# Performance work log

Hardware: AMD Instinct MI355X
Metric: run time of the kernel (lower is better)

The kernel has to match this reference:

```python
import jax, jax.numpy as jnp
import numpy as np

N_HEADS = 16
D_HEAD = 64
D_MODEL = 1024
CHUNK = 64
SCALE = 1.0 / np.sqrt(D_HEAD).astype(np.float32)


def binarize(x):
    # {-1,+1} with straight-through gradient (identity in bwd)
    return x + jax.lax.stop_gradient(jnp.where(x >= 0, 1.0, -1.0).astype(x.dtype) - x)


def setup_inputs() -> dict:
    key = jax.random.key(0)
    k1, k2, k3 = jax.random.split(key, 3)
    B, T, D = 2, 4096, D_MODEL
    x = jax.random.normal(k1, (B, T, D), dtype=jnp.float32)
    w_qkv = jax.random.normal(k2, (3 * D, D), dtype=jnp.float32) * (1.0 / np.sqrt(D))
    w_o = jax.random.normal(k3, (D, D), dtype=jnp.float32) * (1.0 / np.sqrt(D))
    return {"x": x, "w_qkv": w_qkv, "w_o": w_o}


def reference(x, w_qkv, w_o):
    B, T, D = x.shape
    H, d, C = N_HEADS, D_HEAD, CHUNK
    qkv = (x @ w_qkv.T).reshape(B, T, 3, H, d)
    q, k, v = qkv[:, :, 0], qkv[:, :, 1], qkv[:, :, 2]
    # -> (B, H, T, d)
    q = jnp.transpose(q, (0, 2, 1, 3)) * jnp.asarray(SCALE, x.dtype)
    k = binarize(jnp.transpose(k, (0, 2, 1, 3)))
    v = binarize(jnp.transpose(v, (0, 2, 1, 3)))

    assert T % C == 0  # T=4096 divisible by chunk=64 (pad branch not exercised)
    Nc = T // C
    qc = q.reshape(B, H, Nc, C, d)
    kc = k.reshape(B, H, Nc, C, d)
    vc = v.reshape(B, H, Nc, C, d)

    causal_mask = jnp.tril(jnp.ones((C, C), dtype=x.dtype))
    # intra-chunk: (B,H,N,C,C) scores, causal-masked, times values
    intra_scores = jnp.einsum('bhnid,bhnjd->bhnij', qc, kc) * causal_mask
    intra = jnp.einsum('bhnij,bhnjd->bhnid', intra_scores, vc)
    # per-chunk KV outer-product state: (B,H,N,d,d)
    chunk_kv = jnp.einsum('bhntk,bhntv->bhnkv', kc, vc)
    prefix = jnp.cumsum(chunk_kv, axis=2) - chunk_kv  # exclusive prefix
    cross = jnp.einsum('bhnck,bhnkv->bhncv', qc, prefix)
    output = (intra + cross).reshape(B, H, T, d)

    final_state = prefix[:, :, -1] + chunk_kv[:, :, -1]
    out = jnp.transpose(output, (0, 2, 1, 3)).reshape(B, T, D)
    return out @ w_o.T, final_state
```

## Files before the change

### kernel.cpp

```cpp
#include <hip/hip_runtime.h>

typedef __bf16 bf16;
typedef __bf16 bf16x8 __attribute__((ext_vector_type(8)));
typedef _Float16 f16;
typedef _Float16 f16x8 __attribute__((ext_vector_type(8)));
typedef float f32x4 __attribute__((ext_vector_type(4)));

#define SCALE 0.125f
#define AP 72
#define CT 128

__device__ __forceinline__ void async_ld16(const void* g, void* l) {
  __builtin_amdgcn_global_load_lds((const __attribute__((address_space(1))) void*)g,
                                   (__attribute__((address_space(3))) void*)l, 16, 0, 0);
}

__global__ __launch_bounds__(256) void k_convert(
    const float* __restrict__ x, const float* __restrict__ wqkv, const float* __restrict__ wo,
    bf16* __restrict__ xsplit, bf16* __restrict__ wsplit, f16* __restrict__ wo16)
{
  const int N1 = 2097152, N2 = 786432, N3 = 262144;
  const int i = blockIdx.x * 256 + threadIdx.x;
  if (i < N1) {
    f32x4 v = ((const f32x4*)x)[i];
    int e = i * 4, m = e >> 10, c = e & 1023;
    bf16 hi[4], lo[4];
#pragma unroll
    for (int u = 0; u < 4; ++u) { hi[u] = (bf16)v[u]; lo[u] = (bf16)(v[u] - (float)hi[u]); }
    *(ulong1*)&xsplit[(size_t)m * 2048 + c] = *(ulong1*)hi;
    *(ulong1*)&xsplit[(size_t)m * 2048 + 1024 + c] = *(ulong1*)lo;
  } else if (i < N1 + N2) {
    int j = i - N1;
    f32x4 v = ((const f32x4*)wqkv)[j];
    int e = j * 4, n = e >> 10, c = e & 1023;
    bf16 hi[4], lo[4];
#pragma unroll
    for (int u = 0; u < 4; ++u) { hi[u] = (bf16)v[u]; lo[u] = (bf16)(v[u] - (float)hi[u]); }
    *(ulong1*)&wsplit[(size_t)n * 2048 + c] = *(ulong1*)hi;
    *(ulong1*)&wsplit[(size_t)n * 2048 + 1024 + c] = *(ulong1*)lo;
  } else if (i < N1 + N2 + N3) {
    int j = i - N1 - N2;
    f32x4 v = ((const f32x4*)wo)[j];
    f16 h[4];
#pragma unroll
    for (int u = 0; u < 4; ++u) h[u] = (f16)v[u];
    *(ulong1*)&wo16[(size_t)j * 4] = *(ulong1*)h;
  }
}

__global__ __launch_bounds__(256) void k_gemm_qkv(
    const bf16* __restrict__ A, const bf16* __restrict__ B,
    bf16* __restrict__ Qws, bf16* __restrict__ Kws, bf16* __restrict__ Vws)
{
  __shared__ char smem[32768];
  const int tid = threadIdx.x;
  const int wave = tid >> 6, lane = tid & 63;
  const int quad = lane >> 4, l16 = lane & 15;
  const int bxr = (blockIdx.x < 16) ? (blockIdx.x + 8) : (blockIdx.x - 16);
  const int n0 = bxr * 128;
  const int m0 = blockIdx.y * 128;
  const int wm = (wave >> 1) << 6, wn = (wave & 1) << 6;
  const int region = n0 >> 10;
  f32x4 acc[4][4] = {};

  if (region == 0) {
    bf16* As = (bf16*)smem;
    bf16* Bs = As + 128 * 64;
    const int r8 = lane >> 3, c8 = lane & 7;
    const int sw = l16 & 7;
    const int srcoff = (c8 ^ r8) * 8;
    for (int k0 = 0; k0 < 1024; k0 += 64) {
      __syncthreads();
#pragma unroll
      for (int it = 0; it < 4; ++it) {
        const int row = wave * 32 + it * 8 + r8;
        async_ld16(A + (size_t)(m0 + row) * 2048 + k0 + srcoff, As + row * 64 + c8 * 8);
        async_ld16(B + (size_t)(n0 + row) * 2048 + k0 + srcoff, Bs + row * 64 + c8 * 8);
      }
      __syncthreads();
#pragma unroll
      for (int ks = 0; ks < 64; ks += 32) {
        bf16x8 af[4], bg[4];
#pragma unroll
        for (int mi = 0; mi < 4; ++mi)
          af[mi] = *(const bf16x8*)&As[(wm + mi * 16 + l16) * 64 + ((((ks >> 3) + quad) ^ sw) << 3)];
#pragma unroll
        for (int ni = 0; ni < 4; ++ni)
          bg[ni] = *(const bf16x8*)&Bs[(wn + ni * 16 + l16) * 64 + ((((ks >> 3) + quad) ^ sw) << 3)];
#pragma unroll
        for (int mi = 0; mi < 4; ++mi)
#pragma unroll
          for (int ni = 0; ni < 4; ++ni)
            acc[mi][ni] = __builtin_amdgcn_mfma_f32_16x16x32_bf16(af[mi], bg[ni], acc[mi][ni], 0, 0, 0);
      }
    }
  } else {
    bf16* Ah = (bf16*)smem;
    bf16* Al = Ah + 128 * 32;
    bf16* Bh = Al + 128 * 32;
    bf16* Bl = Bh + 128 * 32;
    const int rr0 = tid >> 2;
    const int sl = tid & 3;
    const int rsw = quad ^ (l16 & 3);
    for (int k0 = 0; k0 < 1024; k0 += 32) {
      __syncthreads();
#pragma unroll
      for (int rr = 0; rr < 2; ++rr) {
        const int row = rr * 64 + rr0;
        const int soff = ((sl ^ (row & 3)) << 3);
        const bf16* arow = A + (size_t)(m0 + row) * 2048 + k0 + soff;
        const bf16* brow = B + (size_t)(n0 + row) * 2048 + k0 + soff;
        bf16* ldst = (bf16*)nullptr;
        async_ld16(arow,        Ah + row * 32 + sl * 8);
        async_ld16(arow + 1024, Al + row * 32 + sl * 8);
        async_ld16(brow,        Bh + row * 32 + sl * 8);
        async_ld16(brow + 1024, Bl + row * 32 + sl * 8);
        (void)ldst;
      }
      __syncthreads();
#pragma unroll
      for (int cb = 0; cb < 3; ++cb) {
        const bf16* Asrc = (cb == 1) ? Al : Ah;
        const bf16* Bsrc = (cb == 2) ? Bl : Bh;
        bf16x8 af[4], bg[4];
#pragma unroll
        for (int mi = 0; mi < 4; ++mi)
          af[mi] = *(const bf16x8*)&Asrc[(wm + mi * 16 + l16) * 32 + (rsw << 3)];
#pragma unroll
        for (int ni = 0; ni < 4; ++ni)
          bg[ni] = *(const bf16x8*)&Bsrc[(wn + ni * 16 + l16) * 32 + (rsw << 3)];
#pragma unroll
        for (int mi = 0; mi < 4; ++mi)
#pragma unroll
          for (int ni = 0; ni < 4; ++ni)
            acc[mi][ni] = __builtin_amdgcn_mfma_f32_16x16x32_bf16(af[mi], bg[ni], acc[mi][ni], 0, 0, 0);
      }
    }
  }

  bf16* Ct = (bf16*)smem;
  __syncthreads();
#pragma unroll
  for (int mi = 0; mi < 4; ++mi) {
    const int ml = wm + mi * 16 + quad * 4;
#pragma unroll
    for (int ni = 0; ni < 4; ++ni) {
      const int nl = wn + ni * 16 + l16;
#pragma unroll
      for (int r = 0; r < 4; ++r) {
        const float v = acc[mi][ni][r];
        bf16 o;
        if (region == 0) o = (bf16)(v * SCALE);
        else             o = (bf16)((v >= 0.f) ? 1.f : -1.f);
        Ct[(ml + r) * CT + nl] = o;
      }
    }
  }
  __syncthreads();
  {
    const int row = tid >> 1, half = tid & 1;
    const int nn = (n0 & 1023) + half * 64;
    const int h = nn >> 6;
    const int b = m0 >> 12, t = (m0 & 4095) + row;
    bf16* base = (region == 0) ? Qws : (region == 1) ? Kws : Vws;
    bf16* dst = base + ((size_t)(b * 16 + h) * 4096 + t) * 64;
    const bf16* src = &Ct[row * CT + half * 64];
#pragma unroll
    for (int u = 0; u < 8; ++u)
      *(bf16x8*)(dst + u * 8) = *(const bf16x8*)(src + u * 8);
  }
}

__global__ __launch_bounds__(256) void k_ckv(
    const bf16* __restrict__ Kws, const bf16* __restrict__ Vws, float* __restrict__ ckv)
{
  __shared__ bf16 Kt[64 * AP];
  __shared__ bf16 Vt[64 * AP];
  const int tid = threadIdx.x;
  const int nchunk = blockIdx.x & 63, bh = blockIdx.x >> 6;
  const size_t tbase = ((size_t)bh * 4096 + (size_t)nchunk * 64) * 64;
  const int row = tid >> 2, c0 = (tid & 3) << 4;
  {
    const bf16x8* gk = (const bf16x8*)(Kws + tbase + row * 64 + c0);
    const bf16x8* gv = (const bf16x8*)(Vws + tbase + row * 64 + c0);
    bf16x8 k0 = gk[0], k1 = gk[1], v0 = gv[0], v1 = gv[1];
#pragma unroll
    for (int u = 0; u < 8; ++u) {
      Kt[(c0 + u) * AP + row] = k0[u];
      Kt[(c0 + 8 + u) * AP + row] = k1[u];
      Vt[(c0 + u) * AP + row] = v0[u];
      Vt[(c0 + 8 + u) * AP + row] = v1[u];
    }
  }
  __syncthreads();
  const int wave = tid >> 6, lane = tid & 63;
  const int quad = lane >> 4, l16 = lane & 15;
  const int ti = wave;
  bf16x8 ka[2];
#pragma unroll
  for (int kk = 0; kk < 2; ++kk)
    ka[kk] = *(const bf16x8*)&Kt[(ti * 16 + l16) * AP + kk * 32 + quad * 8];
  float* dst = ckv + ((size_t)bh * 64 + nchunk) * 4096;
#pragma unroll
  for (int td = 0; td < 4; ++td) {
    f32x4 acc = {};
#pragma unroll
    for (int kk = 0; kk < 2; ++kk) {
      const bf16x8 vb = *(const bf16x8*)&Vt[(td * 16 + l16) * AP + kk * 32 + quad * 8];
      acc = __builtin_amdgcn_mfma_f32_16x16x32_bf16(ka[kk], vb, acc, 0, 0, 0);
    }
#pragma unroll
    for (int r = 0; r < 4; ++r)
      dst[(ti * 16 + quad * 4 + r) * 64 + td * 16 + l16] = acc[r];
  }
}

__global__ __launch_bounds__(256) void k_scan(float* __restrict__ ckv, float* __restrict__ fin)
{
  const int idx = blockIdx.x * 256 + threadIdx.x;
  float* p = ckv + ((size_t)(idx >> 12)) * 64 * 4096 + (idx & 4095);
  float run = 0.f;
#pragma unroll
  for (int n = 0; n < 64; ++n) {
    const float v = p[(size_t)n * 4096];
    p[(size_t)n * 4096] = run;
    run += v;
  }
  fin[idx] = run;
}

__global__ __launch_bounds__(256) void k_attn(
    const bf16* __restrict__ Qws, const bf16* __restrict__ Kws, const bf16* __restrict__ Vws,
    const float* __restrict__ pref, f16* __restrict__ attn)
{
  __shared__ bf16 Qs[64 * AP];
  __shared__ bf16 Ks[64 * AP];
  __shared__ bf16 Vt[64 * AP];
  __shared__ bf16 Ph[64 * AP];
  __shared__ bf16 Pl[64 * AP];
  __shared__ bf16 Ss[64 * AP];
  const int tid = threadIdx.x;
  const int blk = blockIdx.x;
  const int nchunk = blk & 63, bh = blk >> 6;
  const int b = bh >> 4, h = bh & 15;
  const size_t tbase = ((size_t)bh * 4096 + (size_t)nchunk * 64) * 64;
  const int row = tid >> 2, c0 = (tid & 3) << 4;
  {
    const bf16x8* gq = (const bf16x8*)(Qws + tbase + row * 64 + c0);
    *(bf16x8*)&Qs[row * AP + c0] = gq[0];
    *(bf16x8*)&Qs[row * AP + c0 + 8] = gq[1];
    const bf16x8* gk = (const bf16x8*)(Kws + tbase + row * 64 + c0);
    *(bf16x8*)&Ks[row * AP + c0] = gk[0];
    *(bf16x8*)&Ks[row * AP + c0 + 8] = gk[1];
    const bf16x8* gv = (const bf16x8*)(Vws + tbase + row * 64 + c0);
    bf16x8 v0 = gv[0], v1 = gv[1];
#pragma unroll
    for (int u = 0; u < 8; ++u) {
      Vt[(c0 + u) * AP + row] = v0[u];
      Vt[(c0 + 8 + u) * AP + row] = v1[u];
    }
    const float* gp = pref + ((size_t)bh * 64 + nchunk) * 4096 + row * 64 + c0;
#pragma unroll
    for (int u = 0; u < 16; ++u) {
      const float p = gp[u];
      const bf16 hi = (bf16)p;
      Ph[(c0 + u) * AP + row] = hi;
      Pl[(c0 + u) * AP + row] = (bf16)(p - (float)hi);
    }
  }
  __syncthreads();

  const int wave = tid >> 6, lane = tid & 63;
  const int quad = lane >> 4, l16 = lane & 15;
  const int ti = wave;

  bf16x8 qa[2];
#pragma unroll
  for (int kk = 0; kk < 2; ++kk)
    qa[kk] = *(const bf16x8*)&Qs[(ti * 16 + l16) * AP + kk * 32 + quad * 8];

  f32x4 sacc[4] = {};
#pragma unroll
  for (int tj = 0; tj < 4; ++tj)
#pragma unroll
    for (int kk = 0; kk < 2; ++kk) {
      const bf16x8 kb = *(const bf16x8*)&Ks[(tj * 16 + l16) * AP + kk * 32 + quad * 8];
      sacc[tj] = __builtin_amdgcn_mfma_f32_16x16x32_bf16(qa[kk], kb, sacc[tj], 0, 0, 0);
    }
#pragma unroll
  for (int tj = 0; tj < 4; ++tj)
#pragma unroll
    for (int r = 0; r < 4; ++r) {
      const int i = ti * 16 + quad * 4 + r;
      const int jj = tj * 16 + l16;
      Ss[i * AP + jj] = (bf16)((jj <= i) ? sacc[tj][r] : 0.f);
    }
  __syncthreads();

  bf16x8 sa[2];
#pragma unroll
  for (int kk = 0; kk < 2; ++kk)
    sa[kk] = *(const bf16x8*)&Ss[(ti * 16 + l16) * AP + kk * 32 + quad * 8];
  f32x4 oacc[4] = {};
#pragma unroll
  for (int td = 0; td < 4; ++td) {
#pragma unroll
    for (int kk = 0; kk < 2; ++kk) {
      const bf16x8 vb = *(const bf16x8*)&Vt[(td * 16 + l16) * AP + kk * 32 + quad * 8];
      oacc[td] = __builtin_amdgcn_mfma_f32_16x16x32_bf16(sa[kk], vb, oacc[td], 0, 0, 0);
    }
#pragma unroll
    for (int kk = 0; kk < 2; ++kk) {
      const bf16x8 pb = *(const bf16x8*)&Ph[(td * 16 + l16) * AP + kk * 32 + quad * 8];
      oacc[td] = __builtin_amdgcn_mfma_f32_16x16x32_bf16(qa[kk], pb, oacc[td], 0, 0, 0);
      const bf16x8 pb2 = *(const bf16x8*)&Pl[(td * 16 + l16) * AP + kk * 32 + quad * 8];
      oacc[td] = __builtin_amdgcn_mfma_f32_16x16x32_bf16(qa[kk], pb2, oacc[td], 0, 0, 0);
    }
  }
  __syncthreads();
  f16* Os = (f16*)Ss;
#pragma unroll
  for (int td = 0; td < 4; ++td)
#pragma unroll
    for (int r = 0; r < 4; ++r) {
      const int i = ti * 16 + quad * 4 + r;
      const int dd = td * 16 + l16;
      Os[i * AP + dd] = (f16)oacc[td][r];
    }
  __syncthreads();
  {
    const int i2 = tid >> 2, q4 = tid & 3;
    const int t = nchunk * 64 + i2;
    f16* dst = attn + ((size_t)(b * 4096 + t)) * 1024 + h * 64 + q4 * 16;
    const f16* src = &Os[i2 * AP + q4 * 16];
    *(f16x8*)(dst) = *(const f16x8*)(src);
    *(f16x8*)(dst + 8) = *(const f16x8*)(src + 8);
  }
}

__global__ __launch_bounds__(256) void k_gemm_out(
    const f16* __restrict__ A, const f16* __restrict__ B, float* __restrict__ out)
{
  __shared__ f16 As[128 * 64];
  __shared__ f16 Bs[128 * 64];
  const int tid = threadIdx.x;
  const int wave = tid >> 6, lane = tid & 63;
  const int quad = lane >> 4, l16 = lane & 15;
  const int n0 = blockIdx.x * 128;
  const int m0 = blockIdx.y * 128;
  const int wm = (wave >> 1) << 6, wn = (wave & 1) << 6;
  const int r8 = lane >> 3, c8 = lane & 7;
  const int sw = l16 & 7;
  const int srcoff = (c8 ^ r8) * 8;
  f32x4 acc[4][4] = {};

  for (int k0 = 0; k0 < 1024; k0 += 64) {
    __syncthreads();
#pragma unroll
    for (int it = 0; it < 4; ++it) {
      const int row = wave * 32 + it * 8 + r8;
      async_ld16(A + (size_t)(m0 + row) * 1024 + k0 + srcoff, As + row * 64 + c8 * 8);
      async_ld16(B + (size_t)(n0 + row) * 1024 + k0 + srcoff, Bs + row * 64 + c8 * 8);
    }
    __syncthreads();
#pragma unroll
    for (int ks = 0; ks < 64; ks += 32) {
      f16x8 af[4], bg[4];
#pragma unroll
      for (int mi = 0; mi < 4; ++mi)
        af[mi] = *(const f16x8*)&As[(wm + mi * 16 + l16) * 64 + ((((ks >> 3) + quad) ^ sw) << 3)];
#pragma unroll
      for (int ni = 0; ni < 4; ++ni)
        bg[ni] = *(const f16x8*)&Bs[(wn + ni * 16 + l16) * 64 + ((((ks >> 3) + quad) ^ sw) << 3)];
#pragma unroll
      for (int mi = 0; mi < 4; ++mi)
#pragma unroll
        for (int ni = 0; ni < 4; ++ni)
          acc[mi][ni] = __builtin_amdgcn_mfma_f32_16x16x32_f16(af[mi], bg[ni], acc[mi][ni], 0, 0, 0);
    }
  }
#pragma unroll
  for (int mi = 0; mi < 4; ++mi)
#pragma unroll
    for (int ni = 0; ni < 4; ++ni)
#pragma unroll
      for (int r = 0; r < 4; ++r) {
        const int m = m0 + wm + mi * 16 + quad * 4 + r;
        const int n = n0 + wn + ni * 16 + l16;
        out[(size_t)m * 1024 + n] = acc[mi][ni][r];
      }
}

extern "C" void kernel_launch(void* const* d_in, const int* in_sizes, int n_in,
                              void* d_out, int out_size, void* d_ws, size_t ws_size,
                              hipStream_t stream)
{
  const float* x = (const float*)d_in[0];
  const float* wqkv = (const float*)d_in[1];
  const float* wo = (const float*)d_in[2];
  float* out = (float*)d_out;
  char* ws = (char*)d_ws;

  bf16* xsplit = (bf16*)(ws);
  bf16* wsplit = (bf16*)(ws + 33554432);
  f16*  wo16   = (f16*)(ws + 46137344);
  bf16* Qws    = (bf16*)(ws + 48234496);
  bf16* Kws    = (bf16*)(ws + 65011712);
  bf16* Vws    = (bf16*)(ws + 81788928);
  float* ckv   = (float*)(ws + 98566144);
  f16*  attn   = (f16*)(ws + 132120576);
  float* fin   = out + 8388608;

  k_convert<<<12288, 256, 0, stream>>>(x, wqkv, wo, xsplit, wsplit, wo16);
  k_gemm_qkv<<<dim3(24, 64), 256, 0, stream>>>(xsplit, wsplit, Qws, Kws, Vws);
  k_ckv<<<2048, 256, 0, stream>>>(Kws, Vws, ckv);
  k_scan<<<512, 256, 0, stream>>>(ckv, fin);
  k_attn<<<2048, 256, 0, stream>>>(Qws, Kws, Vws, ckv, attn);
  k_gemm_out<<<dim3(8, 64), 256, 0, stream>>>(attn, wo16, out);
}
```

Measured before the change: 296.4 us.

## Store chunk KV states as int16 and reuse Q smem for scores

Since K and V are binarized to ±1, per-chunk KV outer products are exact integers bounded by 64, so chunk states are stored as int16 and the prefix scan runs in integer arithmetic. This halves ckv traffic in the ckv, scan and attention kernels. The attention kernel also aliases the score buffer onto the Q shared-memory tile after an extra barrier, lowering LDS use. The QKV GEMM swizzle is changed to XOR on row>>1 to reduce LDS bank conflicts. A risk is int16 overflow of the prefix, which can reach 63*64=4032 and so fits.

```diff
diff --git a/kernel.cpp b/kernel.cpp
--- a/kernel.cpp
+++ b/kernel.cpp
@@ -5,6 +5,7 @@
 typedef _Float16 f16;
 typedef _Float16 f16x8 __attribute__((ext_vector_type(8)));
 typedef float f32x4 __attribute__((ext_vector_type(4)));
+typedef short s16x8 __attribute__((ext_vector_type(8)));
 
 #define SCALE 0.125f
 #define AP 72
@@ -101,21 +102,19 @@
     bf16* Bl = Bh + 128 * 32;
     const int rr0 = tid >> 2;
     const int sl = tid & 3;
-    const int rsw = quad ^ (l16 & 3);
+    const int rsw = quad ^ ((l16 >> 1) & 3);
     for (int k0 = 0; k0 < 1024; k0 += 32) {
       __syncthreads();
 #pragma unroll
       for (int rr = 0; rr < 2; ++rr) {
         const int row = rr * 64 + rr0;
-        const int soff = ((sl ^ (row & 3)) << 3);
+        const int soff = ((sl ^ ((row >> 1) & 3)) << 3);
         const bf16* arow = A + (size_t)(m0 + row) * 2048 + k0 + soff;
         const bf16* brow = B + (size_t)(n0 + row) * 2048 + k0 + soff;
-        bf16* ldst = (bf16*)nullptr;
         async_ld16(arow,        Ah + row * 32 + sl * 8);
         async_ld16(arow + 1024, Al + row * 32 + sl * 8);
         async_ld16(brow,        Bh + row * 32 + sl * 8);
         async_ld16(brow + 1024, Bl + row * 32 + sl * 8);
-        (void)ldst;
       }
       __syncthreads();
 #pragma unroll
@@ -172,7 +171,7 @@
 }
 
 __global__ __launch_bounds__(256) void k_ckv(
-    const bf16* __restrict__ Kws, const bf16* __restrict__ Vws, float* __restrict__ ckv)
+    const bf16* __restrict__ Kws, const bf16* __restrict__ Vws, short* __restrict__ ckv)
 {
   __shared__ bf16 Kt[64 * AP];
   __shared__ bf16 Vt[64 * AP];
@@ -200,7 +199,7 @@
 #pragma unroll
   for (int kk = 0; kk < 2; ++kk)
     ka[kk] = *(const bf16x8*)&Kt[(ti * 16 + l16) * AP + kk * 32 + quad * 8];
-  float* dst = ckv + ((size_t)bh * 64 + nchunk) * 4096;
+  short* dst = ckv + ((size_t)bh * 64 + nchunk) * 4096;
 #pragma unroll
   for (int td = 0; td < 4; ++td) {
     f32x4 acc = {};
@@ -211,34 +210,33 @@
     }
 #pragma unroll
     for (int r = 0; r < 4; ++r)
-      dst[(ti * 16 + quad * 4 + r) * 64 + td * 16 + l16] = acc[r];
-  }
-}
-
-__global__ __launch_bounds__(256) void k_scan(float* __restrict__ ckv, float* __restrict__ fin)
+      dst[(ti * 16 + quad * 4 + r) * 64 + td * 16 + l16] = (short)acc[r];
+  }
+}
+
+__global__ __launch_bounds__(256) void k_scan(short* __restrict__ ckv, float* __restrict__ fin)
 {
   const int idx = blockIdx.x * 256 + threadIdx.x;
-  float* p = ckv + ((size_t)(idx >> 12)) * 64 * 4096 + (idx & 4095);
-  float run = 0.f;
+  short* p = ckv + ((size_t)(idx >> 12)) * 64 * 4096 + (idx & 4095);
+  int run = 0;
 #pragma unroll
   for (int n = 0; n < 64; ++n) {
-    const float v = p[(size_t)n * 4096];
-    p[(size_t)n * 4096] = run;
+    const int v = p[(size_t)n * 4096];
+    p[(size_t)n * 4096] = (short)run;
     run += v;
   }
-  fin[idx] = run;
+  fin[idx] = (float)run;
 }
 
 __global__ __launch_bounds__(256) void k_attn(
     const bf16* __restrict__ Qws, const bf16* __restrict__ Kws, const bf16* __restrict__ Vws,
-    const float* __restrict__ pref, f16* __restrict__ attn)
+    const short* __restrict__ pref, f16* __restrict__ attn)
 {
   __shared__ bf16 Qs[64 * AP];
   __shared__ bf16 Ks[64 * AP];
   __shared__ bf16 Vt[64 * AP];
   __shared__ bf16 Ph[64 * AP];
   __shared__ bf16 Pl[64 * AP];
-  __shared__ bf16 Ss[64 * AP];
   const int tid = threadIdx.x;
   const int blk = blockIdx.x;
   const int nchunk = blk & 63, bh = blk >> 6;
@@ -259,13 +257,23 @@
       Vt[(c0 + u) * AP + row] = v0[u];
       Vt[(c0 + 8 + u) * AP + row] = v1[u];
     }
-    const float* gp = pref + ((size_t)bh * 64 + nchunk) * 4096 + row * 64 + c0;
-#pragma unroll
-    for (int u = 0; u < 16; ++u) {
-      const float p = gp[u];
-      const bf16 hi = (bf16)p;
-      Ph[(c0 + u) * AP + row] = hi;
-      Pl[(c0 + u) * AP + row] = (bf16)(p - (float)hi);
+    const short* gp = pref + ((size_t)bh * 64 + nchunk) * 4096 + row * 64 + c0;
+    s16x8 p0 = *(const s16x8*)(gp);
+    s16x8 p1 = *(const s16x8*)(gp + 8);
+#pragma unroll
+    for (int u = 0; u < 8; ++u) {
+      {
+        const float p = (float)p0[u];
+        const bf16 hi = (bf16)p;
+        Ph[(c0 + u) * AP + row] = hi;
+        Pl[(c0 + u) * AP + row] = (bf16)(p - (float)hi);
+      }
+      {
+        const float p = (float)p1[u];
+        const bf16 hi = (bf16)p;
+        Ph[(c0 + 8 + u) * AP + row] = hi;
+        Pl[(c0 + 8 + u) * AP + row] = (bf16)(p - (float)hi);
+      }
     }
   }
   __syncthreads();
@@ -278,6 +286,9 @@
 #pragma unroll
   for (int kk = 0; kk < 2; ++kk)
     qa[kk] = *(const bf16x8*)&Qs[(ti * 16 + l16) * AP + kk * 32 + quad * 8];
+  __syncthreads();
+
+  bf16* Ss = Qs;
 
   f32x4 sacc[4] = {};
 #pragma unroll
@@ -407,7 +418,7 @@
   bf16* Qws    = (bf16*)(ws + 48234496);
   bf16* Kws    = (bf16*)(ws + 65011712);
   bf16* Vws    = (bf16*)(ws + 81788928);
-  float* ckv   = (float*)(ws + 98566144);
+  short* ckv   = (short*)(ws + 98566144);
   f16*  attn   = (f16*)(ws + 132120576);
   float* fin   = out + 8388608;
 
```

Measured after the change: 283.9 us. 4.2% less time.
